# Optimization experiments

Measured on AMD Instinct MI355X. Metric: run time of the kernel, lower is better.

## Reference

```python
import jax, jax.numpy as jnp
import numpy as np

B, N, C = 8, 1024, 768
H = 12
HD = C // H
STAGES = 3
MLP_H = 4 * C
EPS = 1e-5


def _layernorm(x, w, b):
    mu = jnp.mean(x, axis=-1, keepdims=True)
    var = jnp.mean(jnp.square(x - mu), axis=-1, keepdims=True)
    return (x - mu) * jax.lax.rsqrt(var + EPS) * w + b


def setup_inputs() -> dict:
    key = jax.random.key(0)
    ks = jax.random.split(key, 16)
    s = 0.02
    return {
        "x": jax.random.normal(ks[0], (B, N, C), dtype=jnp.float32),
        # stacked per-stage attention params (torch Linear layout: [out, in])
        "qkv_w": jax.random.normal(ks[1], (STAGES, 3 * C, C), dtype=jnp.float32) * s,
        "proj_w": jax.random.normal(ks[2], (STAGES, C, C), dtype=jnp.float32) * s,
        "proj_b": jnp.zeros((STAGES, C), dtype=jnp.float32),
        "ln1_w": jnp.ones((C,), dtype=jnp.float32),
        "ln1_b": jnp.zeros((C,), dtype=jnp.float32),
        "ln2_w": jnp.ones((C,), dtype=jnp.float32),
        "ln2_b": jnp.zeros((C,), dtype=jnp.float32),
        "mlp_w1": jax.random.normal(ks[3], (MLP_H, C), dtype=jnp.float32) * s,
        "mlp_b1": jnp.zeros((MLP_H,), dtype=jnp.float32),
        "mlp_w2": jax.random.normal(ks[4], (C, MLP_H), dtype=jnp.float32) * s,
        "mlp_b2": jnp.zeros((C,), dtype=jnp.float32),
        "focus_w": jnp.ones((STAGES,), dtype=jnp.float32),
    }


def reference(x, qkv_w, proj_w, proj_b, ln1_w, ln1_b, ln2_w, ln2_b,
              mlp_w1, mlp_b1, mlp_w2, mlp_b2, focus_w):
    scale = HD ** -0.5
    h = _layernorm(x, ln1_w, ln1_b)  # shared norm1(x) input to all stages
    attn_out = jnp.zeros_like(x)
    for i in range(STAGES):
        qkv = jnp.einsum('bnc,oc->bno', h, qkv_w[i])  # [B,N,3C], no bias (qkv_bias=False)
        qkv = qkv.reshape(B, N, 3, H, HD).transpose(2, 0, 3, 1, 4)  # [3,B,H,N,HD]
        q, k, v = qkv[0], qkv[1], qkv[2]
        attn = jax.nn.softmax(jnp.einsum('bhnd,bhmd->bhnm', q, k) * scale, axis=-1)
        o = jnp.einsum('bhnm,bhmd->bhnd', attn, v)  # [B,H,N,HD]
        o = o.transpose(0, 2, 1, 3).reshape(B, N, C)
        o = jnp.einsum('bnc,oc->bno', o, proj_w[i]) + proj_b[i]
        attn_out = attn_out + focus_w[i] * o
    x = x + attn_out
    h2 = _layernorm(x, ln2_w, ln2_b)
    h2 = jax.nn.gelu(jnp.einsum('bnc,hc->bnh', h2, mlp_w1) + mlp_b1, approximate=False)
    mlp_out = jnp.einsum('bnh,ch->bnc', h2, mlp_w2) + mlp_b2
    return x + mlp_out
```

## Files before the change

kernel.cpp:

```cpp
#include <hip/hip_runtime.h>
#include <hip/hip_bf16.h>
#include <math.h>

#define B_    8
#define N_    1024
#define C_    768
#define H_    12
#define HD_   64
#define MLPH_ 3072
#define M_ROWS 8192
#define QKV3  6912
#define PK    2304

typedef float  f32x4   __attribute__((ext_vector_type(4)));
typedef float  f32x16  __attribute__((ext_vector_type(16)));
typedef __bf16 bf16x8  __attribute__((ext_vector_type(8)));

__device__ __forceinline__ f32x4 mfma16(bf16x8 a, bf16x8 b, f32x4 c) {
    return __builtin_amdgcn_mfma_f32_16x16x32_bf16(a, b, c, 0, 0, 0);
}
__device__ __forceinline__ f32x16 mfma32(bf16x8 a, bf16x8 b, f32x16 c) {
    return __builtin_amdgcn_mfma_f32_32x32x16_bf16(a, b, c, 0, 0, 0);
}

__device__ __forceinline__ void gl16(const __bf16* g, __bf16* l) {
    __builtin_amdgcn_global_load_lds(
        (const __attribute__((address_space(1))) unsigned int*)g,
        (__attribute__((address_space(3))) unsigned int*)l,
        16, 0, 0);
}

__device__ __forceinline__ unsigned packbf(float a, float b) {
    __bf16 x = (__bf16)a, y = (__bf16)b;
    union { __bf16 h; unsigned short u; } ux, uy;
    ux.h = x; uy.h = y;
    return (unsigned)ux.u | ((unsigned)uy.u << 16);
}

__global__ __launch_bounds__(256) void cast_f32_bf16(const float* __restrict__ in,
                                                     __bf16* __restrict__ out, int n) {
    int i = blockIdx.x * 256 + threadIdx.x;
    if (i < n) out[i] = (__bf16)in[i];
}

__global__ __launch_bounds__(256) void prep_proj_w(const float* __restrict__ pw,
                                                   const float* __restrict__ focus,
                                                   __bf16* __restrict__ out) {
    int i = blockIdx.x * 256 + threadIdx.x;
    int c = i % C_;
    int s = (i / C_) % 3;
    int o = i / PK;
    out[i] = (__bf16)(focus[s] * pw[((size_t)s * C_ + o) * C_ + c]);
}

__global__ __launch_bounds__(256) void ln_to_bf16(const float* __restrict__ x,
                                                  const float* __restrict__ g,
                                                  const float* __restrict__ bta,
                                                  __bf16* __restrict__ out) {
    int row = blockIdx.x;
    const float* xr = x + (size_t)row * C_;
    int t = threadIdx.x;
    float v0 = xr[t], v1 = xr[t + 256], v2 = xr[t + 512];
    float s  = v0 + v1 + v2;
    float s2 = v0 * v0 + v1 * v1 + v2 * v2;
#pragma unroll
    for (int m = 1; m < 64; m <<= 1) { s += __shfl_xor(s, m); s2 += __shfl_xor(s2, m); }
    __shared__ float red[8];
    int w = t >> 6, lane = t & 63;
    if (lane == 0) { red[w] = s; red[4 + w] = s2; }
    __syncthreads();
    s  = red[0] + red[1] + red[2] + red[3];
    s2 = red[4] + red[5] + red[6] + red[7];
    float mu   = s * (1.f / C_);
    float var  = s2 * (1.f / C_) - mu * mu;
    float rstd = rsqrtf(var + 1e-5f);
    __bf16* orow = out + (size_t)row * C_;
    orow[t]       = (__bf16)((v0 - mu) * rstd * g[t]       + bta[t]);
    orow[t + 256] = (__bf16)((v1 - mu) * rstd * g[t + 256] + bta[t + 256]);
    orow[t + 512] = (__bf16)((v2 - mu) * rstd * g[t + 512] + bta[t + 512]);
}

template <int MODE>
__global__ __launch_bounds__(512, 2) void gemm8(
    const __bf16* __restrict__ A, const __bf16* __restrict__ W,
    int M, int N, int K, int ntn,
    __bf16* __restrict__ obf, const float* __restrict__ bias)
{
    __shared__ __bf16 L[2][2][2][16][512];

    const int t = threadIdx.x, lane = t & 63, w = t >> 6;
    const int wm = w >> 2, wn = w & 3;
    const int lo = lane & 15, hi = lane >> 4;

    const int nwg = gridDim.x;
    const int bid = blockIdx.x;
    const int wgid = (bid & 7) * (nwg >> 3) + (bid >> 3);
    const int m0 = (wgid / ntn) * 256, n0 = (wgid % ntn) * 256;

    const int r16 = lane >> 2;
    const int cc  = ((lane & 3) * 8) ^ ((lane >> 1) & 16);

    auto stage = [&](int buf, int kh, int k0) {
        __bf16* la = &L[buf][0][kh][2 * w][0];
        const size_t ra = (size_t)(m0 + 2 * w * 16 + r16) * K + k0 + cc;
        gl16(&A[ra], la);
        gl16(&A[ra + (size_t)16 * K], la + 512);
        __bf16* lb = &L[buf][1][kh][2 * w][0];
        const size_t rb = (size_t)(n0 + 2 * w * 16 + r16) * K + k0 + cc;
        gl16(&W[rb], lb);
        gl16(&W[rb + (size_t)16 * K], lb + 512);
    };

    const int rdoff = lo * 32 + ((hi * 8) ^ ((lo << 1) & 16));

    const int nkt = K >> 6;
    stage(0, 0, 0);
    stage(0, 1, 32);

    f32x4 acc[8][4] = {};

    for (int kt = 0; kt < nkt; ++kt) {
        const int buf = kt & 1;
#pragma unroll
        for (int kh = 0; kh < 2; ++kh) {
            if (kt == nkt - 1 && kh == 1) asm volatile("s_waitcnt vmcnt(0)" ::: "memory");
            else                          asm volatile("s_waitcnt vmcnt(4)" ::: "memory");
            __builtin_amdgcn_s_barrier();
            __builtin_amdgcn_sched_barrier(0);
            if (kt + 1 < nkt) stage(buf ^ 1, kh, (kt + 1) * 64 + kh * 32);

            bf16x8 af[8], bfr[4];
#pragma unroll
            for (int mf = 0; mf < 8; mf++)
                af[mf] = *(const bf16x8*)&L[buf][0][kh][wm * 8 + mf][rdoff];
#pragma unroll
            for (int nf = 0; nf < 4; nf++)
                bfr[nf] = *(const bf16x8*)&L[buf][1][kh][wn * 4 + nf][rdoff];
            asm volatile("s_waitcnt lgkmcnt(0)" ::: "memory");
            __builtin_amdgcn_sched_barrier(0);
            __builtin_amdgcn_s_setprio(1);
#pragma unroll
            for (int mf = 0; mf < 8; mf++)
#pragma unroll
                for (int nf = 0; nf < 4; nf++)
                    acc[mf][nf] = mfma16(af[mf], bfr[nf], acc[mf][nf]);
            __builtin_amdgcn_s_setprio(0);
        }
    }

#pragma unroll
    for (int mf = 0; mf < 8; mf++) {
#pragma unroll
        for (int nf = 0; nf < 4; nf++) {
            const int col = n0 + wn * 64 + nf * 16 + lo;
#pragma unroll
            for (int r = 0; r < 4; r++) {
                const int row = m0 + wm * 128 + mf * 16 + hi * 4 + r;
                const size_t o = (size_t)row * N + col;
                float v = acc[mf][nf][r];
                if (MODE == 0) {
                    obf[o] = (__bf16)v;
                } else {
                    float u = v + bias[col];
                    float ge = 0.5f * u * (1.0f + erff(u * 0.70710678118654752f));
                    obf[o] = (__bf16)ge;
                }
            }
        }
    }
}

template <int MODE>
__global__ __launch_bounds__(256) void gemm_bt(
    const __bf16* __restrict__ A, const __bf16* __restrict__ W,
    int M, int N, int K,
    __bf16* __restrict__ obf, float* __restrict__ of32,
    const float* __restrict__ resid, const float* __restrict__ bias,
    const float* __restrict__ focus_p)
{
    __shared__ __bf16 As[3][128][32];
    __shared__ __bf16 Bs[3][128][32];

    const int t    = threadIdx.x;
    const int lane = t & 63;
    const int w    = t >> 6;
    const int wr   = w >> 1, wc = w & 1;
    const int m0   = blockIdx.y * 128, n0 = blockIdx.x * 128;
    const int lo   = lane & 15;

    const int srow = lane >> 2;
    const int scol = (((lane & 3) ^ ((lane >> 3) & 3))) * 8;
    const int rcol = ((((lane >> 4) & 3) ^ ((lane >> 1) & 3))) * 8;

    auto stage = [&](int buf, int k0) {
#pragma unroll
        for (int i = 0; i < 2; i++) {
            const int chunk = w * 2 + i;
            const int row   = chunk * 16 + srow;
            gl16(&A[(size_t)(m0 + row) * K + k0 + scol], &As[buf][chunk * 16][0]);
            gl16(&W[(size_t)(n0 + row) * K + k0 + scol], &Bs[buf][chunk * 16][0]);
        }
    };

    const int nT = K >> 5;
    stage(0, 0);
    stage(1, 32);
    stage(2, 64);

    f32x4 acc[4][4] = {};
    int cur = 0;
    for (int tt = 0; tt < nT; ++tt) {
        const int rem = nT - tt;
        if (rem > 2)       asm volatile("s_waitcnt vmcnt(8)" ::: "memory");
        else if (rem == 2) asm volatile("s_waitcnt vmcnt(4)" ::: "memory");
        else               asm volatile("s_waitcnt vmcnt(0)" ::: "memory");
        __builtin_amdgcn_s_barrier();
        __builtin_amdgcn_sched_barrier(0);

        bf16x8 af[4], bfr[4];
#pragma unroll
        for (int mi = 0; mi < 4; mi++) af[mi]  = *(const bf16x8*)&As[cur][wr * 64 + mi * 16 + lo][rcol];
#pragma unroll
        for (int ni = 0; ni < 4; ni++) bfr[ni] = *(const bf16x8*)&Bs[cur][wc * 64 + ni * 16 + lo][rcol];
#pragma unroll
        for (int mi = 0; mi < 4; mi++)
#pragma unroll
            for (int ni = 0; ni < 4; ni++)
                acc[mi][ni] = mfma16(af[mi], bfr[ni], acc[mi][ni]);

        asm volatile("s_waitcnt lgkmcnt(0)" ::: "memory");
        __builtin_amdgcn_s_barrier();
        if (tt + 3 < nT) stage(cur, (tt + 3) * 32);
        cur = (cur == 2) ? 0 : cur + 1;
    }

    float f0 = 0.f, f1 = 0.f, f2 = 0.f;
    if (MODE == 1) { f0 = focus_p[0]; f1 = focus_p[1]; f2 = focus_p[2]; }

#pragma unroll
    for (int mi = 0; mi < 4; mi++) {
#pragma unroll
        for (int ni = 0; ni < 4; ni++) {
            int col = n0 + wc * 64 + ni * 16 + lo;
#pragma unroll
            for (int r = 0; r < 4; r++) {
                int row = m0 + wr * 64 + mi * 16 + (lane >> 4) * 4 + r;
                size_t o = (size_t)row * N + col;
                float v = acc[mi][ni][r];
                if (MODE == 1) {
                    float be = f0 * bias[col] + f1 * bias[col + C_] + f2 * bias[col + 2 * C_];
                    of32[o] = resid[o] + v + be;
                } else {
                    of32[o] = resid[o] + v + bias[col];
                }
            }
        }
    }
}

__global__ __launch_bounds__(256) void attn_kernel(const __bf16* __restrict__ qkv,
                                                   __bf16* __restrict__ obuf) {
    const int bid  = blockIdx.x;
    const int idx  = bid >> 3;
    const int grp  = (bid & 7) * 36 + (idx >> 3);
    const int qt   = idx & 7;
    const int s    = grp / 96;
    const int rem  = grp % 96;
    const int b    = rem / 12;
    const int h    = rem % 12;
    const int q0   = qt * 128;

    const int t = threadIdx.x, lane = t & 63, w = t >> 6;
    const int l31 = lane & 31, hi1 = lane >> 5;

    __shared__ __bf16 Kf[4096];
    __shared__ __bf16 Vf[4096];
    __shared__ float  Lsm[128];

    const size_t rs = QKV3;
    const __bf16* qb = qkv + (size_t)b * N_ * rs + (size_t)s * PK + h * HD_;
    const __bf16* kb = qb + C_;
    const __bf16* vb = qb + 2 * C_;

    const float cexp = 0.18033688011112042f;

    bf16x8 aq[4];
#pragma unroll
    for (int dk = 0; dk < 4; dk++) {
        aq[dk] = *(const bf16x8*)(qb + (size_t)(q0 + w * 32 + l31) * rs + dk * 16 + hi1 * 8);
#pragma unroll
        for (int j = 0; j < 8; j++) aq[dk][j] = (__bf16)((float)aq[dk][j] * cexp);
    }

    f32x16 oacc[2] = {};
    float lsum = 0.f;

    int4 kreg[2]; uint4 vreg[2];
    auto load_tile = [&](int k0) {
#pragma unroll
        for (int p = 0; p < 2; p++) {
            int id = p * 256 + t;
            int kr = id >> 3, d0 = (id & 7) * 8;
            kreg[p] = *(const int4*)(kb + (size_t)(k0 + kr) * rs + d0);
            int kr2 = id & 63, d2 = ((id >> 6) * 8);
            vreg[p] = *(const uint4*)(vb + (size_t)(k0 + kr2) * rs + d2);
        }
    };
    load_tile(0);

    for (int kt = 0; kt < 16; kt++) {
        __syncthreads();
#pragma unroll
        for (int p = 0; p < 2; p++) {
            int id = p * 256 + t;
            int chunk = (id & 7) * 64 + (id >> 3);
            int c = chunk ^ (id & 7);
            *(int4*)&Kf[c * 8] = kreg[p];
        }
        {
            int k8 = lane >> 3, par = lane & 1, koff = lane & 6;
#pragma unroll
            for (int p = 0; p < 2; p++) {
                int d2 = ((p * 256 + t) >> 6) * 8;
#pragma unroll
                for (int i = 0; i < 4; i++) {
                    unsigned mw = vreg[p][i];
                    unsigned pw = (unsigned)__builtin_amdgcn_mov_dpp((int)mw, 0xB1, 0xF, 0xF, true);
                    unsigned out = par ? ((pw >> 16) | (mw & 0xFFFF0000u))
                                       : ((mw & 0xFFFFu) | (pw << 16));
                    int d = d2 + 2 * i + par;
                    int chunk = k8 * 64 + d;
                    int c = chunk ^ k8;
                    *(unsigned*)&Vf[c * 8 + koff] = out;
                }
            }
        }
        __syncthreads();
        if (kt < 15) load_tile((kt + 1) * 64);

        f32x16 sacc[2] = {};
#pragma unroll
        for (int ks = 0; ks < 2; ks++)
#pragma unroll
            for (int dk = 0; dk < 4; dk++) {
                int d8 = dk * 2 + hi1;
                int c = (d8 * 64 + ks * 32 + l31) ^ d8;
                bf16x8 kf = *(const bf16x8*)&Kf[c * 8];
                sacc[ks] = mfma32(kf, aq[dk], sacc[ks]);
            }

#pragma unroll
        for (int ks = 0; ks < 2; ks++) {
            float pe[16];
#pragma unroll
            for (int r = 0; r < 16; r++) {
                pe[r] = __builtin_amdgcn_exp2f(sacc[ks][r]);
                lsum += pe[r];
            }
            unsigned pk[8];
#pragma unroll
            for (int i = 0; i < 8; i++) pk[i] = packbf(pe[2 * i], pe[2 * i + 1]);

            unsigned a0 = pk[0], a2 = pk[2], a1 = pk[1], a3 = pk[3];
            {
                auto r0 = __builtin_amdgcn_permlane32_swap((int)a0, (int)a2, false, false);
                a0 = (unsigned)r0[0]; a2 = (unsigned)r0[1];
                auto r1 = __builtin_amdgcn_permlane32_swap((int)a1, (int)a3, false, false);
                a1 = (unsigned)r1[0]; a3 = (unsigned)r1[1];
            }
            unsigned b0 = pk[4], b2 = pk[6], b1 = pk[5], b3 = pk[7];
            {
                auto r0 = __builtin_amdgcn_permlane32_swap((int)b0, (int)b2, false, false);
                b0 = (unsigned)r0[0]; b2 = (unsigned)r0[1];
                auto r1 = __builtin_amdgcn_permlane32_swap((int)b1, (int)b3, false, false);
                b1 = (unsigned)r1[0]; b3 = (unsigned)r1[1];
            }
            union { unsigned u[4]; bf16x8 v; } fr0, fr1;
            fr0.u[0] = a0; fr0.u[1] = a1; fr0.u[2] = a2; fr0.u[3] = a3;
            fr1.u[0] = b0; fr1.u[1] = b1; fr1.u[2] = b2; fr1.u[3] = b3;

#pragma unroll
            for (int f = 0; f < 2; f++) {
                bf16x8 pa = f ? fr1.v : fr0.v;
#pragma unroll
                for (int dh = 0; dh < 2; dh++) {
                    int k8 = ks * 4 + f * 2 + hi1;
                    int c = (k8 * 64 + dh * 32 + l31) ^ k8;
                    bf16x8 vf = *(const bf16x8*)&Vf[c * 8];
                    oacc[dh] = mfma32(pa, vf, oacc[dh]);
                }
            }
        }
    }

    float ls2 = lsum + __shfl_xor(lsum, 32);
    if (lane < 32) Lsm[w * 32 + lane] = ls2;
    f32x4 Ls[4];
#pragma unroll
    for (int g = 0; g < 4; g++)
        Ls[g] = *(const f32x4*)&Lsm[w * 32 + 8 * g + 4 * hi1];

    __bf16* obase = obuf + ((size_t)b * N_ + q0 + w * 32) * PK + (size_t)s * C_ + h * HD_ + l31;
#pragma unroll
    for (int g = 0; g < 4; g++)
#pragma unroll
        for (int i = 0; i < 4; i++) {
            float inv = 1.0f / Ls[g][i];
            int q_local = i + 8 * g + 4 * hi1;
            __bf16* orow = obase + (size_t)q_local * PK;
            orow[0]  = (__bf16)(oacc[0][4 * g + i] * inv);
            orow[32] = (__bf16)(oacc[1][4 * g + i] * inv);
        }
}

extern "C" void kernel_launch(void* const* d_in, const int* in_sizes, int n_in,
                              void* d_out, int out_size, void* d_ws, size_t ws_size,
                              hipStream_t stream) {
    const float* x      = (const float*)d_in[0];
    const float* qkv_w  = (const float*)d_in[1];
    const float* proj_w = (const float*)d_in[2];
    const float* proj_b = (const float*)d_in[3];
    const float* ln1_w  = (const float*)d_in[4];
    const float* ln1_b  = (const float*)d_in[5];
    const float* ln2_w  = (const float*)d_in[6];
    const float* ln2_b  = (const float*)d_in[7];
    const float* mlp_w1 = (const float*)d_in[8];
    const float* mlp_b1 = (const float*)d_in[9];
    const float* mlp_w2 = (const float*)d_in[10];
    const float* mlp_b2 = (const float*)d_in[11];
    const float* focus  = (const float*)d_in[12];
    float* out = (float*)d_out;

    char* ws = (char*)d_ws;
    size_t off = 0;
    auto alloc = [&](size_t bytes) {
        char* p = ws + off;
        off += (bytes + 255) & ~(size_t)255;
        return p;
    };
    __bf16* h1   = (__bf16*)alloc((size_t)M_ROWS * C_ * 2);
    __bf16* qkvb = (__bf16*)alloc((size_t)M_ROWS * QKV3 * 2);
    __bf16* ob   = (__bf16*)alloc((size_t)M_ROWS * PK * 2);
    float*  x1   = (float*) alloc((size_t)M_ROWS * C_ * 4);
    __bf16* wq   = (__bf16*)alloc((size_t)QKV3 * C_ * 2);
    __bf16* wp   = (__bf16*)alloc((size_t)C_ * PK * 2);
    __bf16* w1   = (__bf16*)alloc((size_t)MLPH_ * C_ * 2);
    __bf16* w2   = (__bf16*)alloc((size_t)C_ * MLPH_ * 2);
    if (off > ws_size) return;
    __bf16* h2  = h1;
    __bf16* hid = qkvb;

    const int nq = QKV3 * C_;
    const int np = C_ * PK;
    const int n1 = MLPH_ * C_;
    cast_f32_bf16<<<(nq + 255) / 256, 256, 0, stream>>>(qkv_w, wq, nq);
    prep_proj_w<<<(np + 255) / 256, 256, 0, stream>>>(proj_w, focus, wp);
    cast_f32_bf16<<<(n1 + 255) / 256, 256, 0, stream>>>(mlp_w1, w1, n1);
    cast_f32_bf16<<<(n1 + 255) / 256, 256, 0, stream>>>(mlp_w2, w2, n1);

    ln_to_bf16<<<M_ROWS, 256, 0, stream>>>(x, ln1_w, ln1_b, h1);

    gemm8<0><<<(M_ROWS / 256) * (QKV3 / 256), 512, 0, stream>>>(
        h1, wq, M_ROWS, QKV3, C_, QKV3 / 256, qkvb, nullptr);

    attn_kernel<<<3 * B_ * H_ * (N_ / 128), 256, 0, stream>>>(qkvb, ob);

    gemm_bt<1><<<dim3(C_ / 128, M_ROWS / 128), 256, 0, stream>>>(
        ob, wp, M_ROWS, C_, PK, nullptr, x1, x, proj_b, focus);

    ln_to_bf16<<<M_ROWS, 256, 0, stream>>>(x1, ln2_w, ln2_b, h2);

    gemm8<2><<<(M_ROWS / 256) * (MLPH_ / 256), 512, 0, stream>>>(
        h2, w1, M_ROWS, MLPH_, C_, MLPH_ / 256, hid, mlp_b1);

    gemm_bt<3><<<dim3(C_ / 128, M_ROWS / 128), 256, 0, stream>>>(
        hid, w2, M_ROWS, C_, MLPH_, nullptr, out, x1, mlp_b2, nullptr);
}
```

Baseline: 490.3 us.

## Double attention query tile per block and fuse weight-cast kernels

```diff
diff --git a/kernel.cpp b/kernel.cpp
--- a/kernel.cpp
+++ b/kernel.cpp
@@ -37,20 +37,29 @@
     return (unsigned)ux.u | ((unsigned)uy.u << 16);
 }
 
-__global__ __launch_bounds__(256) void cast_f32_bf16(const float* __restrict__ in,
-                                                     __bf16* __restrict__ out, int n) {
+__global__ __launch_bounds__(256) void prep_weights(
+    const float* __restrict__ qkv_w, const float* __restrict__ proj_w,
+    const float* __restrict__ mlp_w1, const float* __restrict__ mlp_w2,
+    const float* __restrict__ focus,
+    __bf16* __restrict__ wq, __bf16* __restrict__ wp,
+    __bf16* __restrict__ w1, __bf16* __restrict__ w2) {
+    const int nq = QKV3 * C_;
+    const int np = C_ * PK;
+    const int n1 = MLPH_ * C_;
     int i = blockIdx.x * 256 + threadIdx.x;
-    if (i < n) out[i] = (__bf16)in[i];
-}
-
-__global__ __launch_bounds__(256) void prep_proj_w(const float* __restrict__ pw,
-                                                   const float* __restrict__ focus,
-                                                   __bf16* __restrict__ out) {
-    int i = blockIdx.x * 256 + threadIdx.x;
-    int c = i % C_;
-    int s = (i / C_) % 3;
-    int o = i / PK;
-    out[i] = (__bf16)(focus[s] * pw[((size_t)s * C_ + o) * C_ + c]);
+    if (i < nq) { wq[i] = (__bf16)qkv_w[i]; return; }
+    i -= nq;
+    if (i < np) {
+        int c = i % C_;
+        int st = (i / C_) % 3;
+        int o = i / PK;
+        wp[i] = (__bf16)(focus[st] * proj_w[((size_t)st * C_ + o) * C_ + c]);
+        return;
+    }
+    i -= np;
+    if (i < n1) { w1[i] = (__bf16)mlp_w1[i]; return; }
+    i -= n1;
+    w2[i] = (__bf16)mlp_w2[i];
 }
 
 __global__ __launch_bounds__(256) void ln_to_bf16(const float* __restrict__ x,
@@ -260,22 +269,22 @@
 
 __global__ __launch_bounds__(256) void attn_kernel(const __bf16* __restrict__ qkv,
                                                    __bf16* __restrict__ obuf) {
-    const int bid  = blockIdx.x;
-    const int idx  = bid >> 3;
-    const int grp  = (bid & 7) * 36 + (idx >> 3);
-    const int qt   = idx & 7;
-    const int s    = grp / 96;
-    const int rem  = grp % 96;
-    const int b    = rem / 12;
-    const int h    = rem % 12;
-    const int q0   = qt * 128;
+    const int bid = blockIdx.x;
+    const int idx = bid >> 3;
+    const int grp = (bid & 7) * 36 + (idx >> 2);
+    const int qt  = idx & 3;
+    const int s   = grp / 96;
+    const int rem = grp % 96;
+    const int b   = rem / 12;
+    const int h   = rem % 12;
+    const int q0  = qt * 256;
 
     const int t = threadIdx.x, lane = t & 63, w = t >> 6;
     const int l31 = lane & 31, hi1 = lane >> 5;
 
     __shared__ __bf16 Kf[4096];
     __shared__ __bf16 Vf[4096];
-    __shared__ float  Lsm[128];
+    __shared__ float  Lsm[256];
 
     const size_t rs = QKV3;
     const __bf16* qb = qkv + (size_t)b * N_ * rs + (size_t)s * PK + h * HD_;
@@ -284,16 +293,19 @@
 
     const float cexp = 0.18033688011112042f;
 
-    bf16x8 aq[4];
-#pragma unroll
-    for (int dk = 0; dk < 4; dk++) {
-        aq[dk] = *(const bf16x8*)(qb + (size_t)(q0 + w * 32 + l31) * rs + dk * 16 + hi1 * 8);
-#pragma unroll
-        for (int j = 0; j < 8; j++) aq[dk][j] = (__bf16)((float)aq[dk][j] * cexp);
-    }
-
-    f32x16 oacc[2] = {};
-    float lsum = 0.f;
+    bf16x8 aq[2][4];
+#pragma unroll
+    for (int g = 0; g < 2; g++)
+#pragma unroll
+        for (int dk = 0; dk < 4; dk++) {
+            aq[g][dk] = *(const bf16x8*)(qb + (size_t)(q0 + w * 64 + g * 32 + l31) * rs
+                                          + dk * 16 + hi1 * 8);
+#pragma unroll
+            for (int j = 0; j < 8; j++) aq[g][dk][j] = (__bf16)((float)aq[g][dk][j] * cexp);
+        }
+
+    f32x16 oacc[2][2] = {};
+    float lsum[2] = {0.f, 0.f};
 
     int4 kreg[2]; uint4 vreg[2];
     auto load_tile = [&](int k0) {
@@ -338,79 +350,91 @@
         __syncthreads();
         if (kt < 15) load_tile((kt + 1) * 64);
 
-        f32x16 sacc[2] = {};
-#pragma unroll
-        for (int ks = 0; ks < 2; ks++)
+#pragma unroll
+        for (int ks = 0; ks < 2; ks++) {
+            f32x16 sa0 = {}, sa1 = {};
 #pragma unroll
             for (int dk = 0; dk < 4; dk++) {
                 int d8 = dk * 2 + hi1;
                 int c = (d8 * 64 + ks * 32 + l31) ^ d8;
                 bf16x8 kf = *(const bf16x8*)&Kf[c * 8];
-                sacc[ks] = mfma32(kf, aq[dk], sacc[ks]);
-            }
-
-#pragma unroll
-        for (int ks = 0; ks < 2; ks++) {
-            float pe[16];
-#pragma unroll
-            for (int r = 0; r < 16; r++) {
-                pe[r] = __builtin_amdgcn_exp2f(sacc[ks][r]);
-                lsum += pe[r];
-            }
-            unsigned pk[8];
-#pragma unroll
-            for (int i = 0; i < 8; i++) pk[i] = packbf(pe[2 * i], pe[2 * i + 1]);
-
-            unsigned a0 = pk[0], a2 = pk[2], a1 = pk[1], a3 = pk[3];
-            {
-                auto r0 = __builtin_amdgcn_permlane32_swap((int)a0, (int)a2, false, false);
-                a0 = (unsigned)r0[0]; a2 = (unsigned)r0[1];
-                auto r1 = __builtin_amdgcn_permlane32_swap((int)a1, (int)a3, false, false);
-                a1 = (unsigned)r1[0]; a3 = (unsigned)r1[1];
-            }
-            unsigned b0 = pk[4], b2 = pk[6], b1 = pk[5], b3 = pk[7];
-            {
-                auto r0 = __builtin_amdgcn_permlane32_swap((int)b0, (int)b2, false, false);
-                b0 = (unsigned)r0[0]; b2 = (unsigned)r0[1];
-                auto r1 = __builtin_amdgcn_permlane32_swap((int)b1, (int)b3, false, false);
-                b1 = (unsigned)r1[0]; b3 = (unsigned)r1[1];
-            }
-            union { unsigned u[4]; bf16x8 v; } fr0, fr1;
-            fr0.u[0] = a0; fr0.u[1] = a1; fr0.u[2] = a2; fr0.u[3] = a3;
-            fr1.u[0] = b0; fr1.u[1] = b1; fr1.u[2] = b2; fr1.u[3] = b3;
+                sa0 = mfma32(kf, aq[0][dk], sa0);
+                sa1 = mfma32(kf, aq[1][dk], sa1);
+            }
+
+            bf16x8 paf[2][2];
+#pragma unroll
+            for (int g = 0; g < 2; g++) {
+                float pe[16];
+#pragma unroll
+                for (int r = 0; r < 16; r++) {
+                    pe[r] = __builtin_amdgcn_exp2f(g ? sa1[r] : sa0[r]);
+                    lsum[g] += pe[r];
+                }
+                unsigned pk[8];
+#pragma unroll
+                for (int i = 0; i < 8; i++) pk[i] = packbf(pe[2 * i], pe[2 * i + 1]);
+
+                unsigned a0 = pk[0], a2 = pk[2], a1 = pk[1], a3 = pk[3];
+                {
+                    auto r0 = __builtin_amdgcn_permlane32_swap((int)a0, (int)a2, false, false);
+                    a0 = (unsigned)r0[0]; a2 = (unsigned)r0[1];
+                    auto r1 = __builtin_amdgcn_permlane32_swap((int)a1, (int)a3, false, false);
+                    a1 = (unsigned)r1[0]; a3 = (unsigned)r1[1];
+                }
+                unsigned b0 = pk[4], b2 = pk[6], b1 = pk[5], b3 = pk[7];
+                {
+                    auto r0 = __builtin_amdgcn_permlane32_swap((int)b0, (int)b2, false, false);
+                    b0 = (unsigned)r0[0]; b2 = (unsigned)r0[1];
+                    auto r1 = __builtin_amdgcn_permlane32_swap((int)b1, (int)b3, false, false);
+                    b1 = (unsigned)r1[0]; b3 = (unsigned)r1[1];
+                }
+                union { unsigned u[4]; bf16x8 v; } fr0, fr1;
+                fr0.u[0] = a0; fr0.u[1] = a1; fr0.u[2] = a2; fr0.u[3] = a3;
+                fr1.u[0] = b0; fr1.u[1] = b1; fr1.u[2] = b2; fr1.u[3] = b3;
+                paf[g][0] = fr0.v;
+                paf[g][1] = fr1.v;
+            }
 
 #pragma unroll
             for (int f = 0; f < 2; f++) {
-                bf16x8 pa = f ? fr1.v : fr0.v;
+                int k8 = ks * 4 + f * 2 + hi1;
 #pragma unroll
                 for (int dh = 0; dh < 2; dh++) {
-                    int k8 = ks * 4 + f * 2 + hi1;
                     int c = (k8 * 64 + dh * 32 + l31) ^ k8;
                     bf16x8 vf = *(const bf16x8*)&Vf[c * 8];
-                    oacc[dh] = mfma32(pa, vf, oacc[dh]);
-                }
-            }
-        }
-    }
-
-    float ls2 = lsum + __shfl_xor(lsum, 32);
-    if (lane < 32) Lsm[w * 32 + lane] = ls2;
-    f32x4 Ls[4];
-#pragma unroll
-    for (int g = 0; g < 4; g++)
-        Ls[g] = *(const f32x4*)&Lsm[w * 32 + 8 * g + 4 * hi1];
-
-    __bf16* obase = obuf + ((size_t)b * N_ + q0 + w * 32) * PK + (size_t)s * C_ + h * HD_ + l31;
-#pragma unroll
-    for (int g = 0; g < 4; g++)
-#pragma unroll
-        for (int i = 0; i < 4; i++) {
-            float inv = 1.0f / Ls[g][i];
-            int q_local = i + 8 * g + 4 * hi1;
-            __bf16* orow = obase + (size_t)q_local * PK;
-            orow[0]  = (__bf16)(oacc[0][4 * g + i] * inv);
-            orow[32] = (__bf16)(oacc[1][4 * g + i] * inv);
-        }
+                    oacc[0][dh] = mfma32(paf[0][f], vf, oacc[0][dh]);
+                    oacc[1][dh] = mfma32(paf[1][f], vf, oacc[1][dh]);
+                }
+            }
+        }
+    }
+
+#pragma unroll
+    for (int g = 0; g < 2; g++) {
+        float ls2 = lsum[g] + __shfl_xor(lsum[g], 32);
+        if (lane < 32) Lsm[w * 64 + g * 32 + lane] = ls2;
+    }
+#pragma unroll
+    for (int g = 0; g < 2; g++) {
+        f32x4 Ls[4];
+#pragma unroll
+        for (int gg = 0; gg < 4; gg++)
+            Ls[gg] = *(const f32x4*)&Lsm[w * 64 + g * 32 + 8 * gg + 4 * hi1];
+
+        __bf16* obase = obuf + ((size_t)b * N_ + q0 + w * 64 + g * 32) * PK
+                        + (size_t)s * C_ + h * HD_ + l31;
+#pragma unroll
+        for (int gg = 0; gg < 4; gg++)
+#pragma unroll
+            for (int i = 0; i < 4; i++) {
+                float inv = 1.0f / Ls[gg][i];
+                int q_local = i + 8 * gg + 4 * hi1;
+                __bf16* orow = obase + (size_t)q_local * PK;
+                orow[0]  = (__bf16)(oacc[g][0][4 * gg + i] * inv);
+                orow[32] = (__bf16)(oacc[g][1][4 * gg + i] * inv);
+            }
+    }
 }
 
 extern "C" void kernel_launch(void* const* d_in, const int* in_sizes, int n_in,
@@ -450,20 +474,16 @@
     __bf16* h2  = h1;
     __bf16* hid = qkvb;
 
-    const int nq = QKV3 * C_;
-    const int np = C_ * PK;
-    const int n1 = MLPH_ * C_;
-    cast_f32_bf16<<<(nq + 255) / 256, 256, 0, stream>>>(qkv_w, wq, nq);
-    prep_proj_w<<<(np + 255) / 256, 256, 0, stream>>>(proj_w, focus, wp);
-    cast_f32_bf16<<<(n1 + 255) / 256, 256, 0, stream>>>(mlp_w1, w1, n1);
-    cast_f32_bf16<<<(n1 + 255) / 256, 256, 0, stream>>>(mlp_w2, w2, n1);
+    const int ntot = QKV3 * C_ + C_ * PK + 2 * MLPH_ * C_;
+    prep_weights<<<ntot / 256, 256, 0, stream>>>(
+        qkv_w, proj_w, mlp_w1, mlp_w2, focus, wq, wp, w1, w2);
 
     ln_to_bf16<<<M_ROWS, 256, 0, stream>>>(x, ln1_w, ln1_b, h1);
 
     gemm8<0><<<(M_ROWS / 256) * (QKV3 / 256), 512, 0, stream>>>(
         h1, wq, M_ROWS, QKV3, C_, QKV3 / 256, qkvb, nullptr);
 
-    attn_kernel<<<3 * B_ * H_ * (N_ / 128), 256, 0, stream>>>(qkvb, ob);
+    attn_kernel<<<3 * B_ * H_ * (N_ / 256), 256, 0, stream>>>(qkvb, ob);
 
     gemm_bt<1><<<dim3(C_ / 128, M_ROWS / 128), 256, 0, stream>>>(
         ob, wp, M_ROWS, C_, PK, nullptr, x1, x, proj_b, focus);
```

Result: slower. 512.4 us (+4.5%).
